# Performance work log

Hardware: AMD Instinct MI355X
Metric: run time of the kernel (lower is better)

The kernel has to match this reference:

```python
import jax, jax.numpy as jnp
import numpy as np

N = 10000      # nodes per graph
E = 160000     # random edges per graph (plus N self-loops)
IN_DIM = 4096
HID = 64       # num_hidden
H = 8          # heads
C = 5          # num_classes
SLOPE = 0.2    # LeakyReLU negative slope


def gat_conv(x, src, dst, W, al, ar, b, res_W=None):
    """DGL-style GATConv. x:(N,F) -> (N,H,D). Messages flow src->dst,
    edge softmax over in-edges of each dst node."""
    n = x.shape[0]
    h, d = al.shape
    feat = (x @ W).reshape(n, h, d)                      # (N,H,D)
    el = jnp.sum(feat * al, axis=-1)                     # (N,H)
    er = jnp.sum(feat * ar, axis=-1)                     # (N,H)
    e = jax.nn.leaky_relu(el[src] + er[dst], SLOPE)      # (E,H)
    emax = jax.ops.segment_max(e, dst, num_segments=n)   # (N,H) stable softmax
    ex = jnp.exp(e - emax[dst])
    denom = jax.ops.segment_sum(ex, dst, num_segments=n)
    alpha = ex / denom[dst]                              # (E,H)
    out = jax.ops.segment_sum(feat[src] * alpha[..., None], dst, num_segments=n)
    if res_W is not None:
        out = out + (x @ res_W).reshape(n, h, d)         # residual projection
    return out + b.reshape(h, d)


def encoder(x, src, dst, W0, al0, ar0, b0, W1, al1, ar1, b1):
    h0 = jax.nn.elu(gat_conv(x, src, dst, W0, al0, ar0, b0))   # (N,H,D)
    h0 = h0.reshape(h0.shape[0], -1)                           # flatten(1)
    return jax.nn.elu(gat_conv(h0, src, dst, W1, al1, ar1, b1))


def setup_inputs() -> dict:
    key = jax.random.key(0)
    ks = list(jax.random.split(key, 40))
    ki = iter(ks)

    def edges(k):
        k1, k2 = jax.random.split(k)
        loop = jnp.arange(N, dtype=jnp.int32)
        s = jnp.concatenate([jax.random.randint(k1, (E,), 0, N, dtype=jnp.int32), loop])
        d = jnp.concatenate([jax.random.randint(k2, (E,), 0, N, dtype=jnp.int32), loop])
        return s, d

    inp = {}
    for name in ("s0", "s1", "t"):
        s, d = edges(next(ki))
        inp[f"src_{name}"], inp[f"dst_{name}"] = s, d
    inp["features_s0"] = jax.random.normal(next(ki), (N, IN_DIM), jnp.float32)
    inp["features_s1"] = jax.random.normal(next(ki), (N, IN_DIM), jnp.float32)
    inp["features_t"]  = jax.random.normal(next(ki), (N, IN_DIM), jnp.float32)

    def lin(k, fan_in, fan_out):
        return jax.random.normal(k, (fan_in, fan_out), jnp.float32) / np.sqrt(fan_in)

    inp["W0"] = lin(next(ki), IN_DIM, H * HID)
    inp["al0"] = 0.1 * jax.random.normal(next(ki), (H, HID), jnp.float32)
    inp["ar0"] = 0.1 * jax.random.normal(next(ki), (H, HID), jnp.float32)
    inp["b0"] = jnp.zeros((H * HID,), jnp.float32)
    inp["W1"] = lin(next(ki), H * HID, H * HID)
    inp["al1"] = 0.1 * jax.random.normal(next(ki), (H, HID), jnp.float32)
    inp["ar1"] = 0.1 * jax.random.normal(next(ki), (H, HID), jnp.float32)
    inp["b1"] = jnp.zeros((H * HID,), jnp.float32)
    for k_idx in (0, 1):
        inp[f"Wc{k_idx}"] = lin(next(ki), H * HID, H * C)
        inp[f"alc{k_idx}"] = 0.1 * jax.random.normal(next(ki), (H, C), jnp.float32)
        inp[f"arc{k_idx}"] = 0.1 * jax.random.normal(next(ki), (H, C), jnp.float32)
        inp[f"bc{k_idx}"] = jnp.zeros((H * C,), jnp.float32)
        inp[f"rW{k_idx}"] = lin(next(ki), H * HID, H * C)
    inp["num_source"] = 2
    return inp


def reference(features_s0, features_s1, features_t,
              W0, al0, ar0, b0, W1, al1, ar1, b1,
              Wc0, alc0, arc0, bc0, rW0,
              Wc1, alc1, arc1, bc1, rW1,
              src_s0, dst_s0, src_s1, dst_s1, src_t, dst_t,
              num_source):
    enc_p = (W0, al0, ar0, b0, W1, al1, ar1, b1)
    cls_p = [(Wc0, alc0, arc0, bc0, rW0), (Wc1, alc1, arc1, bc1, rW1)]
    feats = [features_s0, features_s1]
    graphs = [(src_s0, dst_s0), (src_s1, dst_s1)]

    # shared-weight encoder on each source graph
    h_s = [encoder(feats[i], graphs[i][0], graphs[i][1], *enc_p)
           for i in range(num_source)]                    # each (N,H,HID)
    # per-source classifiers on their own graphs, mean over heads
    pred_s = []
    for i in range(num_source):
        Wc, alc, arc, bc, rW = cls_p[i]
        s, d = graphs[i]
        logits = gat_conv(h_s[i].reshape(N, -1), s, d, Wc, alc, arc, bc, res_W=rW)
        pred_s.append(logits.mean(axis=1))               # (N,C)
    emb_s = [h.reshape(N, -1) for h in h_s]

    # target: every source classifier applied to the target graph
    h_t = encoder(features_t, src_t, dst_t, *enc_p)
    pred_t = []
    for i in range(num_source):
        Wc, alc, arc, bc, rW = cls_p[i]
        logits = gat_conv(h_t.reshape(N, -1), src_t, dst_t, Wc, alc, arc, bc, res_W=rW)
        pred_t.append(logits.mean(axis=1))
    emb_t = h_t.reshape(N, -1)

    return (pred_s[0], pred_s[1], pred_t[0], pred_t[1], emb_s[0], emb_s[1], emb_t)
```

## Files before the change

kernel.cpp:

```cpp
#include <hip/hip_runtime.h>
#include <stdint.h>

typedef _Float16 f16;
typedef _Float16 f16x2 __attribute__((ext_vector_type(2)));
typedef _Float16 f16x8 __attribute__((ext_vector_type(8)));
typedef float f32x4 __attribute__((ext_vector_type(4)));

#define AS1 __attribute__((address_space(1)))
#define AS3 __attribute__((address_space(3)))

#define NN 10000
#define NP 10112
#define KK0 4096
#define FF 512

__global__ void k_count_b(const int* __restrict__ d0, const int* __restrict__ d1,
                          const int* __restrict__ d2, int E0, int E1, int E2,
                          int nb0, int nb1, int* __restrict__ deg){
  int b = blockIdx.x;
  const int* d; int Eg, base, lb;
  if (b < nb0){ d=d0; Eg=E0; base=0; lb=b; }
  else if (b < nb0+nb1){ d=d1; Eg=E1; base=NN; lb=b-nb0; }
  else { d=d2; Eg=E2; base=2*NN; lb=b-nb0-nb1; }
  int i = lb*256 + threadIdx.x;
  if (i < Eg) atomicAdd(&deg[base + d[i]], 1);
}

__global__ __launch_bounds__(1024) void k_scan_b(const int* __restrict__ deg_all,
    int* __restrict__ rowptr_all, int* __restrict__ cursor_all){
  int g = blockIdx.x;
  const int* deg = deg_all + g*NN;
  int* rowptr = rowptr_all + g*(NN+1);
  int* cursor = cursor_all + g*NN;
  __shared__ int ps[1024];
  int t = threadIdx.x;
  const int CH = 16;
  int i0 = t*CH;
  int sum = 0;
  for (int k=0;k<CH;k++){ int i=i0+k; if (i<NN) sum += deg[i]; }
  ps[t]=sum; __syncthreads();
  for (int off=1; off<1024; off<<=1){
    int v = (t>=off)? ps[t-off] : 0;
    __syncthreads();
    ps[t] += v;
    __syncthreads();
  }
  int run = ps[t]-sum;
  for (int k=0;k<CH;k++){
    int i=i0+k;
    if (i<=NN) rowptr[i]=run;
    if (i<NN){ cursor[i]=run; run += deg[i]; }
  }
}

__global__ void k_fill_b(const int* __restrict__ s0, const int* __restrict__ d0,
                         const int* __restrict__ s1, const int* __restrict__ d1,
                         const int* __restrict__ s2, const int* __restrict__ d2,
                         int E0, int E1, int E2, int nb0, int nb1,
                         int* __restrict__ cursor_all,
                         int* __restrict__ c0, int* __restrict__ c1, int* __restrict__ c2){
  int b = blockIdx.x;
  const int *s, *d; int Eg, lb; int* cur; int* col;
  if (b < nb0){ s=s0; d=d0; Eg=E0; lb=b; cur=cursor_all; col=c0; }
  else if (b < nb0+nb1){ s=s1; d=d1; Eg=E1; lb=b-nb0; cur=cursor_all+NN; col=c1; }
  else { s=s2; d=d2; Eg=E2; lb=b-nb0-nb1; cur=cursor_all+2*NN; col=c2; }
  int i = lb*256 + threadIdx.x;
  if (i >= Eg) return;
  int slot = atomicAdd(&cur[d[i]], 1);
  col[slot] = s[i];
}

__global__ void k_transpose_t(const float* __restrict__ W, f16* __restrict__ WT,
                              int K, int Nc){
  __shared__ float tile[32][33];
  int n0 = blockIdx.x*32, k0 = blockIdx.y*32;
  int tx = threadIdx.x, ty = threadIdx.y;
  #pragma unroll
  for (int i=0;i<32;i+=8)
    tile[ty+i][tx] = W[(long)(k0+ty+i)*Nc + n0+tx];
  __syncthreads();
  #pragma unroll
  for (int i=0;i<32;i+=8)
    WT[(long)(n0+ty+i)*K + k0+tx] = (f16)tile[tx][ty+i];
}

__global__ void k_pack_wc(const float* __restrict__ Wc, const float* __restrict__ rW,
                          f16* __restrict__ WT){
  int idx = blockIdx.x*256 + threadIdx.x;
  if (idx >= 128*512) return;
  int n = idx >> 9; int k = idx & 511;
  float v = 0.f;
  if (n < 40) v = Wc[k*40 + n];
  else if (n < 80) v = rW[k*40 + (n-40)];
  WT[idx] = (f16)v;
}

template<bool CVT>
__global__ __launch_bounds__(512,1) void k_gemmw(
    const void* __restrict__ A0v, const void* __restrict__ A1v, const void* __restrict__ A2v,
    f16* __restrict__ C0, f16* __restrict__ C1, f16* __restrict__ C2,
    const f16* __restrict__ B,
    const float* __restrict__ alp, const float* __restrict__ arp,
    float* __restrict__ elp, float* __restrict__ erp)
{
  constexpr int K = CVT ? KK0 : FF;
  constexpr int nt = K >> 6;
  __shared__ f16 lds[2][36864];

  const int nwg = gridDim.x;
  const int qd = nwg>>3, rd = nwg&7;
  const int xcd = blockIdx.x & 7, bx = blockIdx.x >> 3;
  const int wid = (xcd < rd ? xcd*(qd+1) : rd*(qd+1) + (xcd-rd)*qd) + bx;
  const int task = wid / 158;
  const int tr = wid - task*158;

  f16* C = task==0?C0:(task==1?C1:C2);

  const int t = threadIdx.x;
  const int wave = t >> 6, lane = t & 63;
  const int slot = (lane&7) ^ (lane>>3);
  const int arow = t >> 3;
  const int ak8 = t & 7;

  #define GLDSB(kt, buf) { \
    int ko = (kt)*64; \
    _Pragma("unroll") \
    for (int i=0;i<8;i++){ \
      int br = i*64 + wave*8 + (lane>>3); \
      __builtin_amdgcn_global_load_lds((const AS1 void*)(B + (long)br*K + ko + slot*8), \
          (AS3 void*)(&lds[buf][4096 + i*4096 + wave*512]), 16, 0, 0); \
    } }

  int abyte[2][4], bbyte[2][4];
  #pragma unroll
  for (int ks=0;ks<2;ks++){
    #pragma unroll
    for (int m=0;m<4;m++){
      int row = m*16 + (lane&15);
      abyte[ks][m] = row*128 + (((ks*4 + (lane>>4))*16) ^ ((row&7)<<4));
    }
    #pragma unroll
    for (int n=0;n<4;n++){
      int brow = wave*64 + n*16 + (lane&15);
      bbyte[ks][n] = 8192 + brow*128 + (((ks*4 + (lane>>4))*16) ^ ((brow&7)<<4));
    }
  }

  f32x4 zero4 = {0.f,0.f,0.f,0.f};
  f32x4 acc[4][4];
  #pragma unroll
  for (int m=0;m<4;m++)
    #pragma unroll
    for (int n=0;n<4;n++) acc[m][n] = zero4;

  #define MFMA_TILE(buf) { \
    const char* Ls = (const char*)&lds[buf][0]; \
    _Pragma("unroll") \
    for (int ks=0;ks<2;ks++){ \
      f16x8 af[4], bf[4]; \
      _Pragma("unroll") \
      for (int m=0;m<4;m++) af[m] = *(const f16x8*)(Ls + abyte[ks][m]); \
      _Pragma("unroll") \
      for (int n=0;n<4;n++) bf[n] = *(const f16x8*)(Ls + bbyte[ks][n]); \
      _Pragma("unroll") \
      for (int m=0;m<4;m++) \
        _Pragma("unroll") \
        for (int n=0;n<4;n++) \
          acc[m][n] = __builtin_amdgcn_mfma_f32_16x16x32_f16(af[m], bf[n], acc[m][n], 0, 0, 0); \
    } }

  int cur = 0;
  if constexpr (CVT){
    const float* Af = task==0?(const float*)A0v:(task==1?(const float*)A1v:(const float*)A2v);
    const bool okA = (tr*64 + arow) < NN;
    const float* gA = Af + (long)(okA ? tr*64+arow : 0)*KK0 + ak8*8;
    f32x4 arE0, arE1;

    #define LOADA(kt) { arE0 = *(const f32x4*)(gA + (kt)*64); \
                        arE1 = *(const f32x4*)(gA + (kt)*64 + 4); }
    #define WRITEA(buf) { \
      f16x8 v; \
      _Pragma("unroll") \
      for (int j=0;j<4;j++){ \
        v[j]   = okA ? (f16)arE0[j] : (f16)0.f; \
        v[4+j] = okA ? (f16)arE1[j] : (f16)0.f; \
      } \
      *(f16x8*)(&lds[buf][arow*64 + ((ak8 ^ (arow&7))*8)]) = v; }

    LOADA(0);
    __builtin_amdgcn_sched_barrier(0);
    GLDSB(0, 0);
    __builtin_amdgcn_sched_barrier(0);
    WRITEA(0);
    __builtin_amdgcn_sched_barrier(0);
    LOADA(1);
    __builtin_amdgcn_sched_barrier(0);
    asm volatile("s_waitcnt vmcnt(2) lgkmcnt(0)" ::: "memory");
    __builtin_amdgcn_s_barrier();

    for (int kt=0; kt<nt; kt++){
      if (kt+1 < nt){
        WRITEA(cur^1);
        __builtin_amdgcn_sched_barrier(0);
        GLDSB(kt+1, cur^1);
        __builtin_amdgcn_sched_barrier(0);
      }
      if (kt+2 < nt){
        LOADA(kt+2);
        __builtin_amdgcn_sched_barrier(0);
      }
      MFMA_TILE(cur);
      if (kt+1 < nt){
        __builtin_amdgcn_sched_barrier(0);
        if (kt+2 < nt)
          asm volatile("s_waitcnt vmcnt(2) lgkmcnt(0)" ::: "memory");
        else
          asm volatile("s_waitcnt vmcnt(0) lgkmcnt(0)" ::: "memory");
        __builtin_amdgcn_s_barrier();
      }
      cur ^= 1;
    }
    #undef LOADA
    #undef WRITEA
  } else {
    const f16* Ah = task==0?(const f16*)A0v:(task==1?(const f16*)A1v:(const f16*)A2v);
    const f16* Ab = Ah + (long)tr*64*K;
    const int aslot = ak8 ^ (arow&7);

    #define GLDSA(kt, buf) \
      __builtin_amdgcn_global_load_lds((const AS1 void*)(Ab + (long)arow*K + (kt)*64 + aslot*8), \
          (AS3 void*)(&lds[buf][wave*512]), 16, 0, 0);

    GLDSA(0, 0);
    GLDSB(0, 0);
    __syncthreads();
    for (int kt=0; kt<nt; kt++){
      if (kt+1 < nt){
        GLDSA(kt+1, cur^1);
        GLDSB(kt+1, cur^1);
      }
      MFMA_TILE(cur);
      __syncthreads();
      cur ^= 1;
    }
    #undef GLDSA
  }
  #undef GLDSB
  #undef MFMA_TILE

  #pragma unroll
  for (int m=0;m<4;m++){
    int row0 = tr*64 + m*16 + ((lane>>4)<<2);
    #pragma unroll
    for (int n=0;n<4;n++){
      int col = wave*64 + n*16 + (lane&15);
      #pragma unroll
      for (int q2=0;q2<4;q2++)
        C[(long)(row0+q2)*FF + col] = (f16)acc[m][n][q2];
    }
  }

  {
    const int head = wave;
    const float* alh = alp + head*64;
    const float* arh = arp + head*64;
    float alv[4], arv[4];
    #pragma unroll
    for (int n=0;n<4;n++){ int d = n*16 + (lane&15); alv[n]=alh[d]; arv[n]=arh[d]; }
    float* elo = elp + (long)task*NN*8;
    float* ero = erp + (long)task*NN*8;
    #pragma unroll
    for (int m=0;m<4;m++){
      float e0,e1,e2,e3,r0,r1,r2,r3;
      #pragma unroll
      for (int qq=0;qq<4;qq++){
        float e=0.f, rr=0.f;
        #pragma unroll
        for (int n=0;n<4;n++){ e += acc[m][n][qq]*alv[n]; rr += acc[m][n][qq]*arv[n]; }
        #pragma unroll
        for (int off=1; off<16; off<<=1){ e += __shfl_xor(e, off); rr += __shfl_xor(rr, off); }
        if (qq==0){e0=e;r0=rr;} else if (qq==1){e1=e;r1=rr;} else if (qq==2){e2=e;r2=rr;} else {e3=e;r3=rr;}
      }
      int qq = lane&15;
      if (qq < 4){
        int node = tr*64 + m*16 + ((lane>>4)<<2) + qq;
        if (node < NN){
          float ev = qq==0?e0:(qq==1?e1:(qq==2?e2:e3));
          float rv = qq==0?r0:(qq==1?r1:(qq==2?r2:r3));
          long o = (long)node*8 + head;
          elo[o] = ev;
          ero[o] = rv;
        }
      }
    }
  }
}

struct GemmTasks { const f16* A[4]; const f16* B[4]; f16* C[4]; };

__global__ __launch_bounds__(256,3) void k_gemmb(GemmTasks p, int ntpb, int ntn,
                                                 int Nc, int K){
  __shared__ f16 lds[2][12288];
  const int bid = blockIdx.x;
  const int task = bid / ntpb;
  const int orig = bid - task*ntpb;
  const int q = ntpb >> 3, r = ntpb & 7;
  const int xcd = orig & 7, bx = orig >> 3;
  const int wid = (xcd < r ? xcd*(q+1) : r*(q+1) + (xcd-r)*q) + bx;
  const int tr = wid / ntn, tc = wid - tr*ntn;

  const f16* A = p.A[task];
  const f16* B = p.B[task];
  f16* C = p.C[task];

  const int t = threadIdx.x;
  const int wave = t >> 6, lane = t & 63;
  const int wr = wave >> 1, wc = wave & 1;

  const f16* Ab = A + (long)tr*64*K;
  const f16* Bb = B + (long)tc*128*K;

  const int slot = (lane&7) ^ (lane>>3);
  const int rbase = wave*8 + (lane>>3);

  f32x4 zero4 = {0.f,0.f,0.f,0.f};
  f32x4 acc[2][4];
  #pragma unroll
  for (int m=0;m<2;m++)
    #pragma unroll
    for (int n=0;n<4;n++) acc[m][n] = zero4;

  int abyte[2][2], bbyte[2][4];
  #pragma unroll
  for (int ks=0;ks<2;ks++){
    #pragma unroll
    for (int m=0;m<2;m++){
      int row = wr*32 + m*16 + (lane&15);
      abyte[ks][m] = row*128 + (((ks*4 + (lane>>4))*16) ^ ((row&7)<<4));
    }
    #pragma unroll
    for (int n=0;n<4;n++){
      int brow = wc*64 + n*16 + (lane&15);
      bbyte[ks][n] = 8192 + brow*128 + (((ks*4 + (lane>>4))*16) ^ ((brow&7)<<4));
    }
  }

  const int nt = K >> 6;
  int cur = 0;

  #pragma unroll
  for (int i=0;i<2;i++)
    __builtin_amdgcn_global_load_lds((const AS1 void*)(Ab + (i*32+rbase)*K + slot*8),
        (AS3 void*)(&lds[0][i*2048 + wave*512]), 16, 0, 0);
  #pragma unroll
  for (int i=0;i<4;i++)
    __builtin_amdgcn_global_load_lds((const AS1 void*)(Bb + (i*32+rbase)*K + slot*8),
        (AS3 void*)(&lds[0][4096 + i*2048 + wave*512]), 16, 0, 0);
  __syncthreads();

  for (int kt=0; kt<nt; kt++){
    if (kt+1 < nt){
      int ko = (kt+1)<<6;
      #pragma unroll
      for (int i=0;i<2;i++)
        __builtin_amdgcn_global_load_lds((const AS1 void*)(Ab + ko + (i*32+rbase)*K + slot*8),
            (AS3 void*)(&lds[cur^1][i*2048 + wave*512]), 16, 0, 0);
      #pragma unroll
      for (int i=0;i<4;i++)
        __builtin_amdgcn_global_load_lds((const AS1 void*)(Bb + ko + (i*32+rbase)*K + slot*8),
            (AS3 void*)(&lds[cur^1][4096 + i*2048 + wave*512]), 16, 0, 0);
    }
    const char* Ls = (const char*)&lds[cur][0];
    #pragma unroll
    for (int ks=0;ks<2;ks++){
      f16x8 af[2], bf[4];
      #pragma unroll
      for (int m=0;m<2;m++) af[m] = *(const f16x8*)(Ls + abyte[ks][m]);
      #pragma unroll
      for (int n=0;n<4;n++) bf[n] = *(const f16x8*)(Ls + bbyte[ks][n]);
      #pragma unroll
      for (int m=0;m<2;m++)
        #pragma unroll
        for (int n=0;n<4;n++)
          acc[m][n] = __builtin_amdgcn_mfma_f32_16x16x32_f16(af[m], bf[n], acc[m][n], 0, 0, 0);
    }
    __syncthreads();
    cur ^= 1;
  }

  #pragma unroll
  for (int m=0;m<2;m++){
    int row0 = tr*64 + wr*32 + m*16 + ((lane>>4)<<2);
    #pragma unroll
    for (int n=0;n<4;n++){
      int col = tc*128 + wc*64 + n*16 + (lane&15);
      #pragma unroll
      for (int q2=0;q2<4;q2++)
        C[(long)(row0+q2)*Nc + col] = (f16)acc[m][n][q2];
    }
  }
}

#define MAXD 128

struct AggArgs {
  const int* rp[3]; const int* cs[3];
  const float* el; const float* er;
  const f16* feat[3];
  const float* bias;
  f16* outH[3];
  float* outF[3];
};

__global__ __launch_bounds__(256) void k_agg_b(AggArgs a){
  int b = blockIdx.x;
  int g = b / NN, n = b - g*NN;
  const int* rowptr = a.rp[g];
  const int* colsrc = a.cs[g];
  const float* el = a.el + (long)g*NN*8;
  const f16* featH = a.feat[g];
  int t = threadIdx.x;
  __shared__ float sm[MAXD*8];
  __shared__ int   scol[MAXD];
  __shared__ float red[256];
  __shared__ float inv[8];
  __shared__ float ern[8];
  if (t < 8) ern[t] = a.er[((long)g*NN+n)*8+t];
  __syncthreads();
  int j0 = rowptr[n], deg = rowptr[n+1]-j0;
  {
    int h = t & 7;
    float dsum = 0.f;
    for (int jj = t>>3; jj < deg; jj += 32){
      int s = colsrc[j0+jj];
      float v = el[s*8+h] + ern[h];
      v = (v>0.f)? v : 0.2f*v;
      float ex = __expf(v);
      dsum += ex;
      if (jj < MAXD){
        sm[jj*8+h] = ex;
        if (h==0) scol[jj] = s;
      }
    }
    red[t] = dsum; __syncthreads();
    if (t<128) red[t] += red[t+128]; __syncthreads();
    if (t<64)  red[t] += red[t+64];  __syncthreads();
    if (t<32)  red[t] += red[t+32];  __syncthreads();
    if (t<16)  red[t] += red[t+16];  __syncthreads();
    if (t<8)   inv[t] = 1.0f / (red[t] + red[t+8]);
    __syncthreads();
  }
  int h = t >> 5;
  int c = t*2;
  float a0=0.f, a1=0.f;
  float ivh = inv[h];
  for (int jj=0; jj<deg; jj++){
    int s; float ex;
    if (jj < MAXD){ s = scol[jj]; ex = sm[jj*8+h]; }
    else {
      s = colsrc[j0+jj];
      float v = el[s*8+h] + ern[h];
      v = (v>0.f)? v : 0.2f*v;
      ex = __expf(v);
    }
    float alpha = ex * ivh;
    f16x2 f = *(const f16x2*)(featH + (long)s*FF + c);
    a0 += alpha*(float)f[0];
    a1 += alpha*(float)f[1];
  }
  a0 += a.bias[c]; a1 += a.bias[c+1];
  a0 = (a0>0.f)? a0 : __expf(a0)-1.f;
  a1 = (a1>0.f)? a1 : __expf(a1)-1.f;
  f16x2 o; o[0]=(f16)a0; o[1]=(f16)a1;
  *(f16x2*)(a.outH[g] + (long)n*FF + c) = o;
  float* oF = a.outF[g];
  if (oF){
    oF[(long)n*FF + c]     = a0;
    oF[(long)n*FF + c + 1] = a1;
  }
}

__global__ void k_elerc_b(const f16* __restrict__ fc,
    const float* __restrict__ alc0, const float* __restrict__ arc0,
    const float* __restrict__ alc1, const float* __restrict__ arc1,
    float* __restrict__ el, float* __restrict__ er){
  int idx = blockIdx.x*256 + threadIdx.x;
  if (idx >= 4*NN*8) return;
  int ti = idx / (NN*8);
  int rem = idx - ti*NN*8;
  int n = rem>>3, hh = rem&7;
  const f16* featc = fc + (long)ti*NP*128;
  const float* al = (ti&1) ? alc1 : alc0;
  const float* ar_ = (ti&1) ? arc1 : arc0;
  float a=0.f, bsum=0.f;
  #pragma unroll
  for (int cc=0; cc<5; cc++){
    float v = (float)featc[(long)n*128 + hh*5 + cc];
    a += v*al[hh*5+cc];
    bsum += v*ar_[hh*5+cc];
  }
  el[idx]=a; er[idx]=bsum;
}

struct ClsArgs {
  const int* rp[3]; const int* cs[3];
  const float* el; const float* er;
  const f16* fc;
  const float* bc[2];
  float* pred;
};

__global__ __launch_bounds__(64) void k_cls_b(ClsArgs a){
  int b = blockIdx.x;
  int ti = b / NN, n = b - ti*NN;
  int g = ti<2 ? ti : 2;
  int ci = ti&1;
  const int* rowptr = a.rp[g];
  const int* colsrc = a.cs[g];
  const float* el = a.el + (long)ti*NN*8;
  const f16* featc = a.fc + (long)ti*NP*128;
  const float* bc = a.bc[ci];
  float* pred = a.pred + (long)ti*5*NN;
  int l = threadIdx.x;
  __shared__ float sm[MAXD*8];
  __shared__ int   scol[MAXD];
  __shared__ float inv[8];
  __shared__ float ern[8];
  __shared__ float lg[40];
  if (l<8) ern[l] = a.er[((long)ti*NN+n)*8+l];
  __syncthreads();
  int j0 = rowptr[n], deg = rowptr[n+1]-j0;
  {
    int h = l & 7;
    float dsum = 0.f;
    for (int jj = l>>3; jj < deg; jj += 8){
      int s = colsrc[j0+jj];
      float v = el[s*8+h] + ern[h];
      v = (v>0.f)? v : 0.2f*v;
      float ex = __expf(v);
      dsum += ex;
      if (jj < MAXD){
        sm[jj*8+h] = ex;
        if (h==0) scol[jj] = s;
      }
    }
    dsum += __shfl_xor(dsum, 8);
    dsum += __shfl_xor(dsum, 16);
    dsum += __shfl_xor(dsum, 32);
    if (l<8) inv[l] = 1.0f/dsum;
  }
  __syncthreads();
  if (l<40){
    int h = l/5;
    float ivh = inv[h];
    float acc = 0.f;
    for (int jj=0; jj<deg; jj++){
      int s; float ex;
      if (jj < MAXD){ s = scol[jj]; ex = sm[jj*8+h]; }
      else {
        s = colsrc[j0+jj];
        float v = el[s*8+h] + ern[h];
        v = (v>0.f)? v : 0.2f*v;
        ex = __expf(v);
      }
      acc += ex*ivh * (float)featc[(long)s*128 + l];
    }
    acc += (float)featc[(long)n*128 + 40 + l];
    acc += bc[l];
    lg[l] = acc;
  }
  __syncthreads();
  if (l<5){
    float p=0.f;
    #pragma unroll
    for (int h=0;h<8;h++) p += lg[h*5+l];
    pred[(long)n*5 + l] = p*0.125f;
  }
}

extern "C" void kernel_launch(void* const* d_in, const int* in_sizes, int n_in,
                              void* d_out, int out_size, void* d_ws, size_t ws_size,
                              hipStream_t stream){
  const int* srcs[3] = {(const int*)d_in[0], (const int*)d_in[2], (const int*)d_in[4]};
  const int* dsts[3] = {(const int*)d_in[1], (const int*)d_in[3], (const int*)d_in[5]};
  int E[3] = {in_sizes[0], in_sizes[2], in_sizes[4]};
  const float* X[3] = {(const float*)d_in[6], (const float*)d_in[7], (const float*)d_in[8]};
  const float* W0  = (const float*)d_in[9];
  const float* al0 = (const float*)d_in[10];
  const float* ar0 = (const float*)d_in[11];
  const float* b0  = (const float*)d_in[12];
  const float* W1  = (const float*)d_in[13];
  const float* al1 = (const float*)d_in[14];
  const float* ar1 = (const float*)d_in[15];
  const float* b1  = (const float*)d_in[16];
  const float* Wcv[2] = {(const float*)d_in[17], (const float*)d_in[22]};
  const float* alc[2] = {(const float*)d_in[18], (const float*)d_in[23]};
  const float* arc[2] = {(const float*)d_in[19], (const float*)d_in[24]};
  const float* bcv[2] = {(const float*)d_in[20], (const float*)d_in[25]};
  const float* rWv[2] = {(const float*)d_in[21], (const float*)d_in[26]};

  float* out = (float*)d_out;
  float* embOut[3] = {out+200000, out+200000+(long)NN*FF, out+200000+2L*NN*FF};

  char* w = (char*)d_ws;
  size_t off = 0;
  auto alloc = [&](size_t bytes)->void*{
    void* p = (void*)(w + off);
    off += (bytes + 255) & ~((size_t)255);
    return p;
  };
  f16* W0T = (f16*)alloc((size_t)FF*KK0*2);
  f16* W1T = (f16*)alloc((size_t)FF*FF*2);
  f16* WcT[2] = {(f16*)alloc(128*512*2), (f16*)alloc(128*512*2)};
  f16* feat0H[3], *h0H[3], *feat1H[3], *embH[3];
  for (int g=0;g<3;g++) feat0H[g] = (f16*)alloc((size_t)NP*FF*2);
  for (int g=0;g<3;g++) h0H[g]    = (f16*)alloc((size_t)NP*FF*2);
  for (int g=0;g<3;g++) feat1H[g] = (f16*)alloc((size_t)NP*FF*2);
  for (int g=0;g<3;g++) embH[g]   = (f16*)alloc((size_t)NP*FF*2);
  f16* featc = (f16*)alloc((size_t)4*NP*128*2);
  float* el_e = (float*)alloc((size_t)3*NN*8*4);
  float* er_e = (float*)alloc((size_t)3*NN*8*4);
  float* el_c = (float*)alloc((size_t)4*NN*8*4);
  float* er_c = (float*)alloc((size_t)4*NN*8*4);
  int* deg    = (int*)alloc((size_t)3*NN*4);
  int* cursor = (int*)alloc((size_t)3*NN*4);
  int* rowptr = (int*)alloc((size_t)3*(NN+1)*4);
  int* colsrc[3];
  for (int g=0;g<3;g++) colsrc[g] = (int*)alloc((size_t)E[g]*4);
  (void)ws_size; (void)n_in; (void)out_size;

  int nb[3] = {(E[0]+255)/256, (E[1]+255)/256, (E[2]+255)/256};
  hipMemsetAsync(deg, 0, (size_t)3*NN*4, stream);
  k_count_b<<<nb[0]+nb[1]+nb[2], 256, 0, stream>>>(dsts[0], dsts[1], dsts[2],
      E[0], E[1], E[2], nb[0], nb[1], deg);
  k_scan_b<<<3, 1024, 0, stream>>>(deg, rowptr, cursor);
  k_fill_b<<<nb[0]+nb[1]+nb[2], 256, 0, stream>>>(srcs[0], dsts[0], srcs[1], dsts[1],
      srcs[2], dsts[2], E[0], E[1], E[2], nb[0], nb[1], cursor,
      colsrc[0], colsrc[1], colsrc[2]);

  k_transpose_t<<<dim3(FF/32, KK0/32), dim3(32,8), 0, stream>>>(W0, W0T, KK0, FF);
  k_transpose_t<<<dim3(FF/32, FF/32), dim3(32,8), 0, stream>>>(W1, W1T, FF, FF);
  k_pack_wc<<<(128*512+255)/256, 256, 0, stream>>>(Wcv[0], rWv[0], WcT[0]);
  k_pack_wc<<<(128*512+255)/256, 256, 0, stream>>>(Wcv[1], rWv[1], WcT[1]);

  const int* rp[3] = {rowptr, rowptr+(NN+1), rowptr+2*(NN+1)};

  k_gemmw<true><<<474, 512, 0, stream>>>(X[0], X[1], X[2],
      feat0H[0], feat0H[1], feat0H[2], W0T, al0, ar0, el_e, er_e);
  {
    AggArgs a;
    for (int g=0;g<3;g++){ a.rp[g]=rp[g]; a.cs[g]=colsrc[g]; a.feat[g]=feat0H[g];
                           a.outH[g]=h0H[g]; a.outF[g]=nullptr; }
    a.el = el_e; a.er = er_e; a.bias = b0;
    k_agg_b<<<3*NN, 256, 0, stream>>>(a);
  }

  k_gemmw<false><<<474, 512, 0, stream>>>(h0H[0], h0H[1], h0H[2],
      feat1H[0], feat1H[1], feat1H[2], W1T, al1, ar1, el_e, er_e);
  {
    AggArgs a;
    for (int g=0;g<3;g++){ a.rp[g]=rp[g]; a.cs[g]=colsrc[g]; a.feat[g]=feat1H[g];
                           a.outH[g]=embH[g]; a.outF[g]=embOut[g]; }
    a.el = el_e; a.er = er_e; a.bias = b1;
    k_agg_b<<<3*NN, 256, 0, stream>>>(a);
  }

  {
    GemmTasks p;
    const int tg[4] = {0,1,2,2};
    for (int i=0;i<4;i++){ p.A[i]=embH[tg[i]]; p.B[i]=WcT[i&1]; p.C[i]=featc + (long)i*NP*128; }
    k_gemmb<<<4*158, 256, 0, stream>>>(p, 158, 1, 128, FF);
  }
  k_elerc_b<<<(4*NN*8+255)/256, 256, 0, stream>>>(featc, alc[0], arc[0], alc[1], arc[1], el_c, er_c);
  {
    ClsArgs a;
    for (int g=0;g<3;g++){ a.rp[g]=rp[g]; a.cs[g]=colsrc[g]; }
    a.el = el_c; a.er = er_c; a.fc = featc;
    a.bc[0] = bcv[0]; a.bc[1] = bcv[1];
    a.pred = out;
    k_cls_b<<<4*NN, 64, 0, stream>>>(a);
  }
}
```

Baseline: 615.4 us.

## Double GEMM row tile to 128 so each block reuses weight tile

The wide GEMM kernels now compute 128 rows per block instead of 64. This doubles per-block accumulators and halves the grid from 474 to 237 blocks, so each B (weight) tile loaded into LDS is reused across twice as many A rows. The aim is to cut redundant weight traffic in the dominant 4096-K projection. In exchange it raises register and LDS use and halves the block count, so fewer blocks run on the 256-CU device and occupancy and latency hiding may suffer.

```diff
diff --git a/kernel.cpp b/kernel.cpp
--- a/kernel.cpp
+++ b/kernel.cpp
@@ -105,21 +105,21 @@
 {
   constexpr int K = CVT ? KK0 : FF;
   constexpr int nt = K >> 6;
-  __shared__ f16 lds[2][36864];
+  __shared__ f16 lds[2][40960];
 
   const int nwg = gridDim.x;
   const int qd = nwg>>3, rd = nwg&7;
   const int xcd = blockIdx.x & 7, bx = blockIdx.x >> 3;
   const int wid = (xcd < rd ? xcd*(qd+1) : rd*(qd+1) + (xcd-rd)*qd) + bx;
-  const int task = wid / 158;
-  const int tr = wid - task*158;
+  const int task = wid / 79;
+  const int tr = wid - task*79;
 
   f16* C = task==0?C0:(task==1?C1:C2);
 
   const int t = threadIdx.x;
   const int wave = t >> 6, lane = t & 63;
   const int slot = (lane&7) ^ (lane>>3);
-  const int arow = t >> 3;
+  const int arow0 = t >> 3;
   const int ak8 = t & 7;
 
   #define GLDSB(kt, buf) { \
@@ -128,28 +128,28 @@
     for (int i=0;i<8;i++){ \
       int br = i*64 + wave*8 + (lane>>3); \
       __builtin_amdgcn_global_load_lds((const AS1 void*)(B + (long)br*K + ko + slot*8), \
-          (AS3 void*)(&lds[buf][4096 + i*4096 + wave*512]), 16, 0, 0); \
+          (AS3 void*)(&lds[buf][8192 + i*4096 + wave*512]), 16, 0, 0); \
     } }
 
-  int abyte[2][4], bbyte[2][4];
+  int abyte[2][8], bbyte[2][4];
   #pragma unroll
   for (int ks=0;ks<2;ks++){
     #pragma unroll
-    for (int m=0;m<4;m++){
+    for (int m=0;m<8;m++){
       int row = m*16 + (lane&15);
       abyte[ks][m] = row*128 + (((ks*4 + (lane>>4))*16) ^ ((row&7)<<4));
     }
     #pragma unroll
     for (int n=0;n<4;n++){
       int brow = wave*64 + n*16 + (lane&15);
-      bbyte[ks][n] = 8192 + brow*128 + (((ks*4 + (lane>>4))*16) ^ ((brow&7)<<4));
+      bbyte[ks][n] = 16384 + brow*128 + (((ks*4 + (lane>>4))*16) ^ ((brow&7)<<4));
     }
   }
 
   f32x4 zero4 = {0.f,0.f,0.f,0.f};
-  f32x4 acc[4][4];
-  #pragma unroll
-  for (int m=0;m<4;m++)
+  f32x4 acc[8][4];
+  #pragma unroll
+  for (int m=0;m<8;m++)
     #pragma unroll
     for (int n=0;n<4;n++) acc[m][n] = zero4;
 
@@ -157,35 +157,49 @@
     const char* Ls = (const char*)&lds[buf][0]; \
     _Pragma("unroll") \
     for (int ks=0;ks<2;ks++){ \
-      f16x8 af[4], bf[4]; \
-      _Pragma("unroll") \
-      for (int m=0;m<4;m++) af[m] = *(const f16x8*)(Ls + abyte[ks][m]); \
+      f16x8 bf[4]; \
       _Pragma("unroll") \
       for (int n=0;n<4;n++) bf[n] = *(const f16x8*)(Ls + bbyte[ks][n]); \
       _Pragma("unroll") \
-      for (int m=0;m<4;m++) \
+      for (int m=0;m<8;m++){ \
+        f16x8 af = *(const f16x8*)(Ls + abyte[ks][m]); \
         _Pragma("unroll") \
         for (int n=0;n<4;n++) \
-          acc[m][n] = __builtin_amdgcn_mfma_f32_16x16x32_f16(af[m], bf[n], acc[m][n], 0, 0, 0); \
+          acc[m][n] = __builtin_amdgcn_mfma_f32_16x16x32_f16(af, bf[n], acc[m][n], 0, 0, 0); \
+      } \
     } }
 
   int cur = 0;
   if constexpr (CVT){
     const float* Af = task==0?(const float*)A0v:(task==1?(const float*)A1v:(const float*)A2v);
-    const bool okA = (tr*64 + arow) < NN;
-    const float* gA = Af + (long)(okA ? tr*64+arow : 0)*KK0 + ak8*8;
-    f32x4 arE0, arE1;
-
-    #define LOADA(kt) { arE0 = *(const f32x4*)(gA + (kt)*64); \
-                        arE1 = *(const f32x4*)(gA + (kt)*64 + 4); }
+    const float* gA[2];
+    bool okA[2];
+    #pragma unroll
+    for (int s=0;s<2;s++){
+      int grow = tr*128 + arow0 + s*64;
+      okA[s] = grow < NN;
+      gA[s] = Af + (long)(okA[s] ? grow : 0)*KK0 + ak8*8;
+    }
+    f32x4 arE[2][2];
+
+    #define LOADA(kt) { \
+      _Pragma("unroll") \
+      for (int s=0;s<2;s++){ \
+        arE[s][0] = *(const f32x4*)(gA[s] + (kt)*64); \
+        arE[s][1] = *(const f32x4*)(gA[s] + (kt)*64 + 4); \
+      } }
     #define WRITEA(buf) { \
-      f16x8 v; \
       _Pragma("unroll") \
-      for (int j=0;j<4;j++){ \
-        v[j]   = okA ? (f16)arE0[j] : (f16)0.f; \
-        v[4+j] = okA ? (f16)arE1[j] : (f16)0.f; \
-      } \
-      *(f16x8*)(&lds[buf][arow*64 + ((ak8 ^ (arow&7))*8)]) = v; }
+      for (int s=0;s<2;s++){ \
+        int row = arow0 + s*64; \
+        f16x8 v; \
+        _Pragma("unroll") \
+        for (int j=0;j<4;j++){ \
+          v[j]   = okA[s] ? (f16)arE[s][0][j] : (f16)0.f; \
+          v[4+j] = okA[s] ? (f16)arE[s][1][j] : (f16)0.f; \
+        } \
+        *(f16x8*)(&lds[buf][row*64 + ((ak8 ^ (arow0&7))*8)]) = v; \
+      } }
 
     LOADA(0);
     __builtin_amdgcn_sched_barrier(0);
@@ -195,7 +209,7 @@
     __builtin_amdgcn_sched_barrier(0);
     LOADA(1);
     __builtin_amdgcn_sched_barrier(0);
-    asm volatile("s_waitcnt vmcnt(2) lgkmcnt(0)" ::: "memory");
+    asm volatile("s_waitcnt vmcnt(4) lgkmcnt(0)" ::: "memory");
     __builtin_amdgcn_s_barrier();
 
     for (int kt=0; kt<nt; kt++){
@@ -213,7 +227,7 @@
       if (kt+1 < nt){
         __builtin_amdgcn_sched_barrier(0);
         if (kt+2 < nt)
-          asm volatile("s_waitcnt vmcnt(2) lgkmcnt(0)" ::: "memory");
+          asm volatile("s_waitcnt vmcnt(4) lgkmcnt(0)" ::: "memory");
         else
           asm volatile("s_waitcnt vmcnt(0) lgkmcnt(0)" ::: "memory");
         __builtin_amdgcn_s_barrier();
@@ -224,12 +238,16 @@
     #undef WRITEA
   } else {
     const f16* Ah = task==0?(const f16*)A0v:(task==1?(const f16*)A1v:(const f16*)A2v);
-    const f16* Ab = Ah + (long)tr*64*K;
-    const int aslot = ak8 ^ (arow&7);
-
-    #define GLDSA(kt, buf) \
-      __builtin_amdgcn_global_load_lds((const AS1 void*)(Ab + (long)arow*K + (kt)*64 + aslot*8), \
-          (AS3 void*)(&lds[buf][wave*512]), 16, 0, 0);
+    const f16* Ab = Ah + (long)tr*128*K;
+    const int r8 = lane>>3;
+
+    #define GLDSA(kt, buf) { \
+      _Pragma("unroll") \
+      for (int s=0;s<2;s++){ \
+        int arow = wave*8 + r8 + s*64; \
+        __builtin_amdgcn_global_load_lds((const AS1 void*)(Ab + (long)arow*K + (kt)*64 + slot*8), \
+            (AS3 void*)(&lds[buf][s*4096 + wave*512]), 16, 0, 0); \
+      } }
 
     GLDSA(0, 0);
     GLDSB(0, 0);
@@ -249,8 +267,8 @@
   #undef MFMA_TILE
 
   #pragma unroll
-  for (int m=0;m<4;m++){
-    int row0 = tr*64 + m*16 + ((lane>>4)<<2);
+  for (int m=0;m<8;m++){
+    int row0 = tr*128 + m*16 + ((lane>>4)<<2);
     #pragma unroll
     for (int n=0;n<4;n++){
       int col = wave*64 + n*16 + (lane&15);
@@ -270,7 +288,7 @@
     float* elo = elp + (long)task*NN*8;
     float* ero = erp + (long)task*NN*8;
     #pragma unroll
-    for (int m=0;m<4;m++){
+    for (int m=0;m<8;m++){
       float e0,e1,e2,e3,r0,r1,r2,r3;
       #pragma unroll
       for (int qq=0;qq<4;qq++){
@@ -283,7 +301,7 @@
       }
       int qq = lane&15;
       if (qq < 4){
-        int node = tr*64 + m*16 + ((lane>>4)<<2) + qq;
+        int node = tr*128 + m*16 + ((lane>>4)<<2) + qq;
         if (node < NN){
           float ev = qq==0?e0:(qq==1?e1:(qq==2?e2:e3));
           float rv = qq==0?r0:(qq==1?r1:(qq==2?r2:r3));
@@ -645,7 +663,7 @@
 
   const int* rp[3] = {rowptr, rowptr+(NN+1), rowptr+2*(NN+1)};
 
-  k_gemmw<true><<<474, 512, 0, stream>>>(X[0], X[1], X[2],
+  k_gemmw<true><<<237, 512, 0, stream>>>(X[0], X[1], X[2],
       feat0H[0], feat0H[1], feat0H[2], W0T, al0, ar0, el_e, er_e);
   {
     AggArgs a;
@@ -655,7 +673,7 @@
     k_agg_b<<<3*NN, 256, 0, stream>>>(a);
   }
 
-  k_gemmw<false><<<474, 512, 0, stream>>>(h0H[0], h0H[1], h0H[2],
+  k_gemmw<false><<<237, 512, 0, stream>>>(h0H[0], h0H[1], h0H[2],
       feat1H[0], feat1H[1], feat1H[2], W1T, al1, ar1, el_e, er_e);
   {
     AggArgs a;
```

After: 538.5 us. 1.14x faster.
